# Kernel tuning notes

Measured on AMD Instinct MI355X. Metric: run time of the kernel, lower is better.

## Reference

```python
import jax, jax.numpy as jnp
import numpy as np

EMBED = 1024
HEADS = 16
HEAD_DIM = EMBED // HEADS
SCALE = HEAD_DIM ** -0.5


def setup_inputs() -> dict:
    key = jax.random.key(0)
    ks = jax.random.split(key, 9)
    B, N = 2, 2048
    std = EMBED ** -0.5
    return {
        "query": jax.random.normal(ks[0], (B, N, EMBED), jnp.float32),
        "key": jax.random.normal(ks[1], (B, N, EMBED), jnp.float32),
        "value": jax.random.normal(ks[2], (B, N, EMBED), jnp.float32),
        # torch nn.Linear weights are [out, in]; y = x @ W.T + b
        "Wq": jax.random.normal(ks[3], (EMBED, EMBED), jnp.float32) * std,
        "bq": jax.random.normal(ks[4], (EMBED,), jnp.float32) * 0.01,
        "Wk": jax.random.normal(ks[5], (EMBED, EMBED), jnp.float32) * std,
        "bk": jax.random.normal(ks[6], (EMBED,), jnp.float32) * 0.01,
        "Wv": jax.random.normal(ks[7], (EMBED, EMBED), jnp.float32) * std,
        "bv": jax.random.normal(ks[8], (EMBED,), jnp.float32) * 0.01,
    }


def reference(query, key, value, Wq, bq, Wk, bk, Wv, bv):
    B, NQ, _ = query.shape
    NK = key.shape[1]
    q = query @ Wq.T + bq  # [B, NQ, E]
    k = key @ Wk.T + bk    # [B, NK, E]
    v = value @ Wv.T + bv  # [B, NK, E]
    # split heads -> [B, H, N, Dh]
    q = q.reshape(B, NQ, HEADS, HEAD_DIM).transpose(0, 2, 1, 3)
    k = k.reshape(B, NK, HEADS, HEAD_DIM).transpose(0, 2, 1, 3)
    v = v.reshape(B, NK, HEADS, HEAD_DIM).transpose(0, 2, 1, 3)
    attn = jnp.einsum("bhqd,bhkd->bhqk", q, k) * SCALE  # [B, H, NQ, NK]
    attn = jax.nn.softmax(attn, axis=-1)
    out = jnp.einsum("bhqk,bhkd->bhqd", attn, v)  # [B, H, NQ, Dh]
    out = out.transpose(0, 2, 1, 3).reshape(B, NQ, EMBED)
    # o_proj is Identity (odim == embed_dim, o_proj=False); dropout is 0 (eval)
    return out
```

## Files before the change

### kernel.cpp

```cpp
#include <hip/hip_runtime.h>

#define EMB 1024
#define NSEQ 2048
#define NBATCH 2
#define NHEAD 16
#define DHEAD 64
#define QSCALE 0.18033688011112042f

typedef float f32x4 __attribute__((ext_vector_type(4)));
typedef short s16x8 __attribute__((ext_vector_type(8)));
typedef short s16x4 __attribute__((ext_vector_type(4)));

typedef __attribute__((address_space(3))) short lds_short;
typedef __attribute__((address_space(1))) const short glb_short;

__device__ __forceinline__ void gl_lds16(const short* g, short* l) {
    __builtin_amdgcn_global_load_lds((glb_short*)g, (lds_short*)l, 16, 0, 0);
}

__device__ __forceinline__ short bf16r(float f) {
    unsigned u = __float_as_uint(f);
    u += 0x7fffu + ((u >> 16) & 1u);
    return (short)(u >> 16);
}

__device__ __forceinline__ unsigned pkbf(float a, float b) {
#if defined(__has_builtin) && __has_builtin(__builtin_amdgcn_cvt_pk_bf16_f32)
    auto r = __builtin_amdgcn_cvt_pk_bf16_f32(a, b);
    unsigned u;
    __builtin_memcpy(&u, &r, 4);
    return u;
#else
    return ((unsigned)bf16r(a) & 0xffffu) | ((unsigned)bf16r(b) << 16);
#endif
}

__device__ __forceinline__ float fexp2(float x) {
#if defined(__has_builtin) && __has_builtin(__builtin_amdgcn_exp2f)
    return __builtin_amdgcn_exp2f(x);
#else
    return exp2f(x);
#endif
}

__global__ __launch_bounds__(256) void cvt6_kernel(
    const float* __restrict__ s0, const float* __restrict__ s1, const float* __restrict__ s2,
    const float* __restrict__ s3, const float* __restrict__ s4, const float* __restrict__ s5,
    short* __restrict__ d0, short* __restrict__ d1, short* __restrict__ d2,
    short* __restrict__ d3, short* __restrict__ d4, short* __restrict__ d5,
    int n0, int n1, int n2, int n3, int n4, int n5)
{
    const int seg = blockIdx.y;
    const float* s = (seg == 0) ? s0 : (seg == 1) ? s1 : (seg == 2) ? s2
                   : (seg == 3) ? s3 : (seg == 4) ? s4 : s5;
    short* d = (seg == 0) ? d0 : (seg == 1) ? d1 : (seg == 2) ? d2
             : (seg == 3) ? d3 : (seg == 4) ? d4 : d5;
    const int n = (seg == 0) ? n0 : (seg == 1) ? n1 : (seg == 2) ? n2
                : (seg == 3) ? n3 : (seg == 4) ? n4 : n5;

    const int i = (blockIdx.x * 256 + threadIdx.x) * 8;
    if (i >= n) return;
    float4 a = *(const float4*)(s + i);
    float4 b = *(const float4*)(s + i + 4);
    uint4 u = { pkbf(a.x, a.y), pkbf(a.z, a.w), pkbf(b.x, b.y), pkbf(b.z, b.w) };
    *(uint4*)(d + i) = u;
}

__global__ __launch_bounds__(256, 3) void proj2_kernel(
    const short* __restrict__ Xq, const short* __restrict__ Xk, const short* __restrict__ Xv,
    const short* __restrict__ Wq, const short* __restrict__ Wk, const short* __restrict__ Wv,
    const float* __restrict__ bq, const float* __restrict__ bk, const float* __restrict__ bv,
    short* __restrict__ Oq, short* __restrict__ Ok, short* __restrict__ Ov)
{
    const int z = blockIdx.z;
    const short* X    = (z == 0) ? Xq : (z == 1) ? Xk : Xv;
    const short* W    = (z == 0) ? Wq : (z == 1) ? Wk : Wv;
    const float* bias = (z == 0) ? bq : (z == 1) ? bk : bv;
    short* Out        = (z == 0) ? Oq : (z == 1) ? Ok : Ov;
    const float osc   = (z == 0) ? QSCALE : 1.0f;

    const int n0 = blockIdx.x * 128;
    const int m0 = blockIdx.y * 128;

    __shared__ __align__(16) short As[128 * 64];
    __shared__ __align__(16) short Bs[128 * 64];

    const int t    = threadIdx.x;
    const int lane = t & 63;
    const int wave = t >> 6;
    const int r    = lane & 15;
    const int quad = lane >> 4;
    const int wm   = (wave >> 1) * 64;
    const int wn   = (wave & 1) * 64;

    const int p0    = wave * 256 + lane;
    const int row0  = p0 >> 3;
    const int lc0   = (p0 & 7) ^ (row0 & 7);
    const short* gA = X + (size_t)(m0 + row0) * EMB + lc0 * 8;
    const short* gB = W + (size_t)(n0 + row0) * EMB + lc0 * 8;
    short* lA = As + p0 * 8;
    short* lB = Bs + p0 * 8;

    f32x4 acc[4][4];
#pragma unroll
    for (int i = 0; i < 4; ++i)
#pragma unroll
        for (int j = 0; j < 4; ++j)
#pragma unroll
            for (int v = 0; v < 4; ++v) acc[i][j][v] = 0.f;

    for (int k0 = 0; k0 < EMB; k0 += 64) {
#pragma unroll
        for (int i = 0; i < 4; ++i) {
            gl_lds16(gA + k0 + (size_t)8 * i * EMB, lA + i * 512);
            gl_lds16(gB + k0 + (size_t)8 * i * EMB, lB + i * 512);
        }
        __syncthreads();

#pragma unroll
        for (int ks = 0; ks < 2; ++ks) {
            const int fc = ((ks * 4 + quad) ^ (r & 7)) * 8;
            s16x8 af[4], bf[4];
#pragma unroll
            for (int i = 0; i < 4; ++i) af[i] = *(const s16x8*)&As[(wm + i * 16 + r) * 64 + fc];
#pragma unroll
            for (int j = 0; j < 4; ++j) bf[j] = *(const s16x8*)&Bs[(wn + j * 16 + r) * 64 + fc];
#pragma unroll
            for (int i = 0; i < 4; ++i)
#pragma unroll
                for (int j = 0; j < 4; ++j)
                    acc[i][j] = __builtin_amdgcn_mfma_f32_16x16x32_bf16(af[i], bf[j], acc[i][j], 0, 0, 0);
        }
        __syncthreads();
    }

#pragma unroll
    for (int j = 0; j < 4; ++j) {
        const int gn = n0 + wn + j * 16 + r;
        const float bb = bias[gn];
#pragma unroll
        for (int i = 0; i < 4; ++i)
#pragma unroll
            for (int reg = 0; reg < 4; ++reg) {
                const int gm = m0 + wm + i * 16 + quad * 4 + reg;
                Out[(size_t)gm * EMB + gn] = bf16r((acc[i][j][reg] + bb) * osc);
            }
    }
}

__global__ __launch_bounds__(256) void proj_kernel(
    const float* __restrict__ Xq, const float* __restrict__ Xk, const float* __restrict__ Xv,
    const float* __restrict__ Wq, const float* __restrict__ Wk, const float* __restrict__ Wv,
    const float* __restrict__ bq, const float* __restrict__ bk, const float* __restrict__ bv,
    short* __restrict__ Oq, short* __restrict__ Ok, short* __restrict__ Ov)
{
    const int z = blockIdx.z;
    const float* X    = (z == 0) ? Xq : (z == 1) ? Xk : Xv;
    const float* W    = (z == 0) ? Wq : (z == 1) ? Wk : Wv;
    const float* bias = (z == 0) ? bq : (z == 1) ? bk : bv;
    short* Out        = (z == 0) ? Oq : (z == 1) ? Ok : Ov;
    const float osc   = (z == 0) ? QSCALE : 1.0f;

    const int n0 = blockIdx.x * 128;
    const int m0 = blockIdx.y * 128;

    __shared__ __align__(16) short As[128][40];
    __shared__ __align__(16) short Bs[128][40];

    const int t    = threadIdx.x;
    const int lane = t & 63;
    const int wave = t >> 6;
    const int r    = lane & 15;
    const int quad = lane >> 4;
    const int wm   = (wave >> 1) * 64;
    const int wn   = (wave & 1) * 64;

    const int srow = t >> 1;
    const int scol = (t & 1) << 4;

    f32x4 acc[4][4];
#pragma unroll
    for (int i = 0; i < 4; ++i)
#pragma unroll
        for (int j = 0; j < 4; ++j)
#pragma unroll
            for (int v = 0; v < 4; ++v) acc[i][j][v] = 0.f;

    for (int k0 = 0; k0 < EMB; k0 += 32) {
        const float4* xp = (const float4*)(X + (size_t)(m0 + srow) * EMB + k0 + scol);
        const float4* wp = (const float4*)(W + (size_t)(n0 + srow) * EMB + k0 + scol);
        float4 x0 = xp[0], x1 = xp[1], x2 = xp[2], x3 = xp[3];
        float4 w0 = wp[0], w1 = wp[1], w2 = wp[2], w3 = wp[3];
        uint4 a0 = { pkbf(x0.x, x0.y), pkbf(x0.z, x0.w), pkbf(x1.x, x1.y), pkbf(x1.z, x1.w) };
        uint4 a1 = { pkbf(x2.x, x2.y), pkbf(x2.z, x2.w), pkbf(x3.x, x3.y), pkbf(x3.z, x3.w) };
        uint4 b0 = { pkbf(w0.x, w0.y), pkbf(w0.z, w0.w), pkbf(w1.x, w1.y), pkbf(w1.z, w1.w) };
        uint4 b1 = { pkbf(w2.x, w2.y), pkbf(w2.z, w2.w), pkbf(w3.x, w3.y), pkbf(w3.z, w3.w) };
        *(uint4*)&As[srow][scol]     = a0;
        *(uint4*)&As[srow][scol + 8] = a1;
        *(uint4*)&Bs[srow][scol]     = b0;
        *(uint4*)&Bs[srow][scol + 8] = b1;
        __syncthreads();

        s16x8 af[4], bf[4];
#pragma unroll
        for (int i = 0; i < 4; ++i) af[i] = *(const s16x8*)&As[wm + i * 16 + r][quad * 8];
#pragma unroll
        for (int j = 0; j < 4; ++j) bf[j] = *(const s16x8*)&Bs[wn + j * 16 + r][quad * 8];
#pragma unroll
        for (int i = 0; i < 4; ++i)
#pragma unroll
            for (int j = 0; j < 4; ++j)
                acc[i][j] = __builtin_amdgcn_mfma_f32_16x16x32_bf16(af[i], bf[j], acc[i][j], 0, 0, 0);
        __syncthreads();
    }

#pragma unroll
    for (int j = 0; j < 4; ++j) {
        const int gn = n0 + wn + j * 16 + r;
        const float bb = bias[gn];
#pragma unroll
        for (int i = 0; i < 4; ++i)
#pragma unroll
            for (int reg = 0; reg < 4; ++reg) {
                const int gm = m0 + wm + i * 16 + quad * 4 + reg;
                Out[(size_t)gm * EMB + gn] = bf16r((acc[i][j][reg] + bb) * osc);
            }
    }
}

__global__ __launch_bounds__(256) void vtrans_kernel(
    const short* __restrict__ Vp, short* __restrict__ VT)
{
    const int n0 = blockIdx.x * 64;
    const int h  = blockIdx.y;
    const int b  = blockIdx.z;
    __shared__ __align__(16) short L[64][72];

    const int t  = threadIdx.x;
    const int rr = t >> 2;
    const int cc = (t & 3) * 16;

    const short* src = Vp + (size_t)(b * NSEQ + n0 + rr) * EMB + h * DHEAD + cc;
    s16x8 a = *(const s16x8*)src;
    s16x8 c = *(const s16x8*)(src + 8);
    *(s16x8*)&L[rr][cc]     = a;
    *(s16x8*)&L[rr][cc + 8] = c;
    __syncthreads();

    const int d  = t >> 2;
    const int c4 = (t & 3) * 16;
    short vals[16];
#pragma unroll
    for (int i = 0; i < 16; ++i) vals[i] = L[c4 + i][d];
    short* dst = VT + ((size_t)(b * NHEAD + h) * DHEAD + d) * NSEQ + n0 + c4;
    *(s16x8*)dst       = *(s16x8*)&vals[0];
    *(s16x8*)(dst + 8) = *(s16x8*)&vals[8];
}

__global__ __launch_bounds__(256, 2) void attn7_kernel(
    const short* __restrict__ Qp, const short* __restrict__ Kp,
    const short* __restrict__ VT, float* __restrict__ Out)
{
    const int qblk = blockIdx.x * 128;
    const int h    = blockIdx.y;
    const int b    = blockIdx.z;

    __shared__ __align__(16) char smem[35840];
    short* Ks   = (short*)smem;
    short* Vs   = (short*)smem + 128 * 72;
    float* fbuf = (float*)smem;

    const int t    = threadIdx.x;
    const int lane = t & 63;
    const int w    = t >> 6;
    const int r    = lane & 15;
    const int quad = lane >> 4;

    const size_t rowbase = (size_t)b * NSEQ;
    const int    colbase = h * DHEAD;
    const size_t bh64    = (size_t)(b * NHEAD + h) * DHEAD;

    s16x8 qf[2][2];
#pragma unroll
    for (int qs = 0; qs < 2; ++qs)
#pragma unroll
        for (int ks = 0; ks < 2; ++ks)
            qf[qs][ks] = *(const s16x8*)(Qp + (rowbase + qblk + w * 32 + qs * 16 + r) * EMB
                                          + colbase + ks * 32 + quad * 8);

    f32x4 accO[2][4];
    float lsum[2] = {0.f, 0.f};
#pragma unroll
    for (int qs = 0; qs < 2; ++qs)
#pragma unroll
        for (int dt = 0; dt < 4; ++dt)
#pragma unroll
            for (int v = 0; v < 4; ++v) accO[qs][dt][v] = 0.f;

    const int srk = t >> 1;
    const int sck = (t & 1) * 32;
    const short* gK = Kp + (rowbase + srk) * EMB + colbase + sck;
    short* lK = Ks + srk * 72 + sck;

    const int srv = t >> 2;
    const int scv = (t & 3) * 32;
    const short* gV = VT + (bh64 + srv) * NSEQ + scv;
    short* lV = Vs + srv * 136 + scv;

    s16x8 kr[4], vr[4];
#pragma unroll
    for (int j = 0; j < 4; ++j) {
        kr[j] = *(const s16x8*)(gK + j * 8);
        vr[j] = *(const s16x8*)(gV + j * 8);
    }

    for (int kt = 0; kt < 16; ++kt) {
#pragma unroll
        for (int j = 0; j < 4; ++j) {
            *(s16x8*)(lK + j * 8) = kr[j];
            *(s16x8*)(lV + j * 8) = vr[j];
        }
        __syncthreads();

        if (kt + 1 < 16) {
            const short* gKt = gK + (size_t)(kt + 1) * 128 * EMB;
            const short* gVt = gV + (kt + 1) * 128;
#pragma unroll
            for (int j = 0; j < 4; ++j) {
                kr[j] = *(const s16x8*)(gKt + j * 8);
                vr[j] = *(const s16x8*)(gVt + j * 8);
            }
        }

        s16x8 pf[2][4];
#pragma unroll
        for (int s = 0; s < 4; ++s) {
            s16x8 kf00 = *(const s16x8*)&Ks[((2 * s) * 16 + r) * 72 + quad * 8];
            s16x8 kf01 = *(const s16x8*)&Ks[((2 * s) * 16 + r) * 72 + 32 + quad * 8];
            s16x8 kf10 = *(const s16x8*)&Ks[((2 * s + 1) * 16 + r) * 72 + quad * 8];
            s16x8 kf11 = *(const s16x8*)&Ks[((2 * s + 1) * 16 + r) * 72 + 32 + quad * 8];
#pragma unroll
            for (int qs = 0; qs < 2; ++qs) {
                f32x4 s0, s1;
#pragma unroll
                for (int v = 0; v < 4; ++v) { s0[v] = 0.f; s1[v] = 0.f; }
                s0 = __builtin_amdgcn_mfma_f32_16x16x32_bf16(kf00, qf[qs][0], s0, 0, 0, 0);
                s0 = __builtin_amdgcn_mfma_f32_16x16x32_bf16(kf01, qf[qs][1], s0, 0, 0, 0);
                s1 = __builtin_amdgcn_mfma_f32_16x16x32_bf16(kf10, qf[qs][0], s1, 0, 0, 0);
                s1 = __builtin_amdgcn_mfma_f32_16x16x32_bf16(kf11, qf[qs][1], s1, 0, 0, 0);
                float p0[4], p1[4];
#pragma unroll
                for (int reg = 0; reg < 4; ++reg) {
                    p0[reg] = fexp2(s0[reg]);
                    p1[reg] = fexp2(s1[reg]);
                    lsum[qs] += p0[reg] + p1[reg];
                }
                uint4 uu = { pkbf(p0[0], p0[1]), pkbf(p0[2], p0[3]),
                             pkbf(p1[0], p1[1]), pkbf(p1[2], p1[3]) };
                __builtin_memcpy(&pf[qs][s], &uu, 16);
            }
        }

#pragma unroll
        for (int dt = 0; dt < 4; ++dt) {
            s16x8 vfl[4];
#pragma unroll
            for (int s = 0; s < 4; ++s) {
                s16x4 lo = *(const s16x4*)&Vs[(dt * 16 + r) * 136 + s * 32 + quad * 4];
                s16x4 hi = *(const s16x4*)&Vs[(dt * 16 + r) * 136 + s * 32 + 16 + quad * 4];
                vfl[s] = __builtin_shufflevector(lo, hi, 0, 1, 2, 3, 4, 5, 6, 7);
            }
#pragma unroll
            for (int qs = 0; qs < 2; ++qs)
#pragma unroll
                for (int s = 0; s < 4; ++s)
                    accO[qs][dt] = __builtin_amdgcn_mfma_f32_16x16x32_bf16(vfl[s], pf[qs][s], accO[qs][dt], 0, 0, 0);
        }
        __syncthreads();
    }

    float rl[2];
#pragma unroll
    for (int qs = 0; qs < 2; ++qs) {
        float s = lsum[qs];
        s += __shfl_xor(s, 16);
        s += __shfl_xor(s, 32);
        rl[qs] = 1.f / s;
    }

#pragma unroll
    for (int qs = 0; qs < 2; ++qs) {
        __syncthreads();
#pragma unroll
        for (int dt = 0; dt < 4; ++dt)
#pragma unroll
            for (int reg = 0; reg < 4; ++reg)
                fbuf[(w * 16 + r) * 68 + dt * 16 + quad * 4 + reg] = accO[qs][dt][reg] * rl[qs];
        __syncthreads();
        const int qi   = t >> 2;
        const int c    = (t & 3) * 16;
        const int wsrc = qi >> 4;
        const int rsrc = qi & 15;
        const float4* fp = (const float4*)&fbuf[(wsrc * 16 + rsrc) * 68 + c];
        float4 o0 = fp[0], o1 = fp[1], o2 = fp[2], o3 = fp[3];
        float* op = Out + (rowbase + qblk + wsrc * 32 + qs * 16 + rsrc) * EMB + colbase + c;
        ((float4*)op)[0] = o0;
        ((float4*)op)[1] = o1;
        ((float4*)op)[2] = o2;
        ((float4*)op)[3] = o3;
    }
}

__global__ __launch_bounds__(256) void attn_fb_kernel(
    const short* __restrict__ Qp, const short* __restrict__ Kp,
    const short* __restrict__ Vp, float* __restrict__ Out)
{
    const int qt = blockIdx.x;
    const int h  = blockIdx.y;
    const int b  = blockIdx.z;

    __shared__ __align__(16) short Ks[64][72];
    __shared__ __align__(16) short VsT[64][72];
    __shared__ __align__(16) short Ps[4][16][72];

    const int t    = threadIdx.x;
    const int lane = t & 63;
    const int w    = t >> 6;
    const int r    = lane & 15;
    const int quad = lane >> 4;

    const size_t rowbase = (size_t)b * NSEQ;
    const int colbase    = h * DHEAD;

    const short* Qr = Qp + (rowbase + qt * 64 + w * 16 + r) * EMB + colbase;
    const s16x8 qf0 = *(const s16x8*)(Qr + quad * 8);
    const s16x8 qf1 = *(const s16x8*)(Qr + 32 + quad * 8);

    float mrow[4], lrow[4];
    f32x4 accO[4];
#pragma unroll
    for (int i = 0; i < 4; ++i) {
        mrow[i] = -INFINITY;
        lrow[i] = 0.f;
#pragma unroll
        for (int v = 0; v < 4; ++v) accO[i][v] = 0.f;
    }

    const int srow = t >> 2;
    const int scol = (t & 3) << 4;

    for (int kt = 0; kt < 32; ++kt) {
        const short* Krow = Kp + (rowbase + kt * 64 + srow) * EMB + colbase + scol;
        const short* Vrow = Vp + (rowbase + kt * 64 + srow) * EMB + colbase + scol;
        s16x8 kv0 = *(const s16x8*)Krow;
        s16x8 kv1 = *(const s16x8*)(Krow + 8);
        s16x8 vv0 = *(const s16x8*)Vrow;
        s16x8 vv1 = *(const s16x8*)(Vrow + 8);
        *(s16x8*)&Ks[srow][scol]     = kv0;
        *(s16x8*)&Ks[srow][scol + 8] = kv1;
#pragma unroll
        for (int i = 0; i < 8; ++i) {
            VsT[scol + i][srow]     = vv0[i];
            VsT[scol + 8 + i][srow] = vv1[i];
        }
        __syncthreads();

        f32x4 sacc[4];
#pragma unroll
        for (int j = 0; j < 4; ++j) {
#pragma unroll
            for (int v = 0; v < 4; ++v) sacc[j][v] = 0.f;
            s16x8 kf0 = *(const s16x8*)&Ks[j * 16 + r][quad * 8];
            s16x8 kf1 = *(const s16x8*)&Ks[j * 16 + r][32 + quad * 8];
            sacc[j] = __builtin_amdgcn_mfma_f32_16x16x32_bf16(qf0, kf0, sacc[j], 0, 0, 0);
            sacc[j] = __builtin_amdgcn_mfma_f32_16x16x32_bf16(qf1, kf1, sacc[j], 0, 0, 0);
        }

        float rmax[4];
#pragma unroll
        for (int reg = 0; reg < 4; ++reg) rmax[reg] = -INFINITY;
#pragma unroll
        for (int j = 0; j < 4; ++j)
#pragma unroll
            for (int reg = 0; reg < 4; ++reg)
                rmax[reg] = fmaxf(rmax[reg], sacc[j][reg]);
#pragma unroll
        for (int reg = 0; reg < 4; ++reg) {
#pragma unroll
            for (int mask = 1; mask <= 8; mask <<= 1)
                rmax[reg] = fmaxf(rmax[reg], __shfl_xor(rmax[reg], mask, 64));
        }

        float alpha[4], rsum[4];
#pragma unroll
        for (int reg = 0; reg < 4; ++reg) {
            float mnew = fmaxf(mrow[reg], rmax[reg]);
            alpha[reg] = fexp2(mrow[reg] - mnew);
            mrow[reg]  = mnew;
            rsum[reg]  = 0.f;
        }

#pragma unroll
        for (int j = 0; j < 4; ++j)
#pragma unroll
            for (int reg = 0; reg < 4; ++reg) {
                float p = fexp2(sacc[j][reg] - mrow[reg]);
                rsum[reg] += p;
                Ps[w][quad * 4 + reg][j * 16 + r] = bf16r(p);
            }
#pragma unroll
        for (int reg = 0; reg < 4; ++reg) {
#pragma unroll
            for (int mask = 1; mask <= 8; mask <<= 1)
                rsum[reg] += __shfl_xor(rsum[reg], mask, 64);
            lrow[reg] = lrow[reg] * alpha[reg] + rsum[reg];
        }
#pragma unroll
        for (int j = 0; j < 4; ++j)
#pragma unroll
            for (int reg = 0; reg < 4; ++reg) accO[j][reg] *= alpha[reg];

#pragma unroll
        for (int s = 0; s < 2; ++s) {
            s16x8 pfr = *(const s16x8*)&Ps[w][r][s * 32 + quad * 8];
#pragma unroll
            for (int j = 0; j < 4; ++j) {
                s16x8 vfr = *(const s16x8*)&VsT[j * 16 + r][s * 32 + quad * 8];
                accO[j] = __builtin_amdgcn_mfma_f32_16x16x32_bf16(pfr, vfr, accO[j], 0, 0, 0);
            }
        }
        __syncthreads();
    }

#pragma unroll
    for (int j = 0; j < 4; ++j)
#pragma unroll
        for (int reg = 0; reg < 4; ++reg) {
            const int qrow = qt * 64 + w * 16 + quad * 4 + reg;
            Out[(rowbase + qrow) * EMB + colbase + j * 16 + r] = accO[j][reg] / lrow[reg];
        }
}

extern "C" void kernel_launch(void* const* d_in, const int* in_sizes, int n_in,
                              void* d_out, int out_size, void* d_ws, size_t ws_size,
                              hipStream_t stream) {
    const float* query = (const float*)d_in[0];
    const float* key   = (const float*)d_in[1];
    const float* value = (const float*)d_in[2];
    const float* Wq    = (const float*)d_in[3];
    const float* bq    = (const float*)d_in[4];
    const float* Wk    = (const float*)d_in[5];
    const float* bk    = (const float*)d_in[6];
    const float* Wv    = (const float*)d_in[7];
    const float* bv    = (const float*)d_in[8];
    float* out = (float*)d_out;

    const size_t XBUF = (size_t)NBATCH * NSEQ * EMB;
    const size_t WBUF = (size_t)EMB * EMB;

    short* Qb  = (short*)d_ws;
    short* Kb  = Qb + XBUF;
    short* Vb  = Kb + XBUF;
    short* VTb = Vb + XBUF;
    short* Xqb = VTb + XBUF;
    short* Xkb = Xqb + XBUF;
    short* Xvb = Xkb + XBUF;
    short* Wqb = Xvb + XBUF;
    short* Wkb = Wqb + WBUF;
    short* Wvb = Wkb + WBUF;

    const size_t need_full  = (7 * XBUF + 3 * WBUF) * sizeof(short);
    const size_t need_attn7 = 4 * XBUF * sizeof(short);

    if (ws_size >= need_full) {
        cvt6_kernel<<<dim3(2048, 6), 256, 0, stream>>>(
            query, key, value, Wq, Wk, Wv,
            Xqb, Xkb, Xvb, Wqb, Wkb, Wvb,
            (int)XBUF, (int)XBUF, (int)XBUF, (int)WBUF, (int)WBUF, (int)WBUF);
        proj2_kernel<<<dim3(EMB / 128, (NBATCH * NSEQ) / 128, 3), 256, 0, stream>>>(
            Xqb, Xkb, Xvb, Wqb, Wkb, Wvb, bq, bk, bv, Qb, Kb, Vb);
        vtrans_kernel<<<dim3(NSEQ / 64, NHEAD, NBATCH), 256, 0, stream>>>(Vb, VTb);
        attn7_kernel<<<dim3(NSEQ / 128, NHEAD, NBATCH), 256, 0, stream>>>(Qb, Kb, VTb, out);
    } else if (ws_size >= need_attn7) {
        proj_kernel<<<dim3(EMB / 128, (NBATCH * NSEQ) / 128, 3), 256, 0, stream>>>(
            query, key, value, Wq, Wk, Wv, bq, bk, bv, Qb, Kb, Vb);
        vtrans_kernel<<<dim3(NSEQ / 64, NHEAD, NBATCH), 256, 0, stream>>>(Vb, VTb);
        attn7_kernel<<<dim3(NSEQ / 128, NHEAD, NBATCH), 256, 0, stream>>>(Qb, Kb, VTb, out);
    } else {
        proj_kernel<<<dim3(EMB / 128, (NBATCH * NSEQ) / 128, 3), 256, 0, stream>>>(
            query, key, value, Wq, Wk, Wv, bq, bk, bv, Qb, Kb, Vb);
        attn_fb_kernel<<<dim3(NSEQ / 64, NHEAD, NBATCH), 256, 0, stream>>>(Qb, Kb, Vb, out);
    }
}
```

Before: 205.5 us.

## Fuse V transpose into projection epilogue and widen attention blocks to 512 threads

The projection kernel now writes V directly in the per-head transposed layout, which removes the separate vtrans kernel launch and its extra pass over V. The attention kernel moves to 512 threads, with each wave handling 16 query rows instead of 32, and uses XOR-swizzled LDS layouts for K and V instead of padded rows. It also wraps MFMA groups in s_setprio. The epilogue is simplified to a single pass. The risks are scattered 8-byte stores in the projection epilogue and higher register and occupancy pressure from the 512-thread blocks.

```diff
diff --git a/kernel.cpp b/kernel.cpp
--- a/kernel.cpp
+++ b/kernel.cpp
@@ -134,17 +134,37 @@
         __syncthreads();
     }
 
-#pragma unroll
-    for (int j = 0; j < 4; ++j) {
-        const int gn = n0 + wn + j * 16 + r;
-        const float bb = bias[gn];
-#pragma unroll
-        for (int i = 0; i < 4; ++i)
-#pragma unroll
-            for (int reg = 0; reg < 4; ++reg) {
-                const int gm = m0 + wm + i * 16 + quad * 4 + reg;
-                Out[(size_t)gm * EMB + gn] = bf16r((acc[i][j][reg] + bb) * osc);
+    if (z != 2) {
+#pragma unroll
+        for (int j = 0; j < 4; ++j) {
+            const int gn = n0 + wn + j * 16 + r;
+            const float bb = bias[gn];
+#pragma unroll
+            for (int i = 0; i < 4; ++i)
+#pragma unroll
+                for (int reg = 0; reg < 4; ++reg) {
+                    const int gm = m0 + wm + i * 16 + quad * 4 + reg;
+                    Out[(size_t)gm * EMB + gn] = bf16r((acc[i][j][reg] + bb) * osc);
+                }
+        }
+    } else {
+#pragma unroll
+        for (int j = 0; j < 4; ++j) {
+            const int gn = n0 + wn + j * 16 + r;
+            const float bb = bias[gn];
+            const int hh = gn >> 6;
+            const int dd = gn & 63;
+#pragma unroll
+            for (int i = 0; i < 4; ++i) {
+                const int gm = m0 + wm + i * 16 + quad * 4;
+                const int bi = gm >> 11;
+                const int nn = gm & 2047;
+                s16x4 pk;
+#pragma unroll
+                for (int reg = 0; reg < 4; ++reg) pk[reg] = bf16r(acc[i][j][reg] + bb);
+                *(s16x4*)(Out + ((size_t)(bi * NHEAD + hh) * DHEAD + dd) * NSEQ + nn) = pk;
             }
+        }
     }
 }
 
@@ -257,7 +277,7 @@
     *(s16x8*)(dst + 8) = *(s16x8*)&vals[8];
 }
 
-__global__ __launch_bounds__(256, 2) void attn7_kernel(
+__global__ __launch_bounds__(512, 4) void attn8_kernel(
     const short* __restrict__ Qp, const short* __restrict__ Kp,
     const short* __restrict__ VT, float* __restrict__ Out)
 {
@@ -265,9 +285,9 @@
     const int h    = blockIdx.y;
     const int b    = blockIdx.z;
 
-    __shared__ __align__(16) char smem[35840];
+    __shared__ __align__(16) char smem[34816];
     short* Ks   = (short*)smem;
-    short* Vs   = (short*)smem + 128 * 72;
+    short* Vs   = (short*)smem + 128 * 64;
     float* fbuf = (float*)smem;
 
     const int t    = threadIdx.x;
@@ -275,140 +295,137 @@
     const int w    = t >> 6;
     const int r    = lane & 15;
     const int quad = lane >> 4;
+    const int r7   = r & 7;
 
     const size_t rowbase = (size_t)b * NSEQ;
     const int    colbase = h * DHEAD;
     const size_t bh64    = (size_t)(b * NHEAD + h) * DHEAD;
 
-    s16x8 qf[2][2];
-#pragma unroll
-    for (int qs = 0; qs < 2; ++qs)
-#pragma unroll
-        for (int ks = 0; ks < 2; ++ks)
-            qf[qs][ks] = *(const s16x8*)(Qp + (rowbase + qblk + w * 32 + qs * 16 + r) * EMB
-                                          + colbase + ks * 32 + quad * 8);
-
-    f32x4 accO[2][4];
-    float lsum[2] = {0.f, 0.f};
-#pragma unroll
-    for (int qs = 0; qs < 2; ++qs)
-#pragma unroll
-        for (int dt = 0; dt < 4; ++dt)
-#pragma unroll
-            for (int v = 0; v < 4; ++v) accO[qs][dt][v] = 0.f;
-
-    const int srk = t >> 1;
-    const int sck = (t & 1) * 32;
-    const short* gK = Kp + (rowbase + srk) * EMB + colbase + sck;
-    short* lK = Ks + srk * 72 + sck;
-
-    const int srv = t >> 2;
-    const int scv = (t & 3) * 32;
-    const short* gV = VT + (bh64 + srv) * NSEQ + scv;
-    short* lV = Vs + srv * 136 + scv;
-
-    s16x8 kr[4], vr[4];
-#pragma unroll
-    for (int j = 0; j < 4; ++j) {
-        kr[j] = *(const s16x8*)(gK + j * 8);
-        vr[j] = *(const s16x8*)(gV + j * 8);
-    }
+    const short* qrow = Qp + (rowbase + qblk + w * 16 + r) * EMB + colbase;
+    const s16x8 qf0 = *(const s16x8*)(qrow + quad * 8);
+    const s16x8 qf1 = *(const s16x8*)(qrow + 32 + quad * 8);
+
+    f32x4 accO[4];
+#pragma unroll
+    for (int dt = 0; dt < 4; ++dt)
+#pragma unroll
+        for (int v = 0; v < 4; ++v) accO[dt][v] = 0.f;
+    float lsum0 = 0.f, lsum1 = 0.f;
+    const f32x4 zf = {0.f, 0.f, 0.f, 0.f};
+
+    const int krow = t >> 2;
+    const int kc   = (t & 3) * 2;
+    const int kcs  = kc ^ (krow & 7);
+    const short* gK = Kp + (rowbase + krow) * EMB + colbase + kc * 8;
+    short* lK0 = Ks + krow * 64 + kcs * 8;
+    short* lK1 = Ks + krow * 64 + (kcs ^ 1) * 8;
+
+    const int vrow = t >> 3;
+    const int vc   = (t & 7) * 2;
+    const int vcs  = vc ^ (vrow & 7);
+    const short* gV = VT + (bh64 + vrow) * NSEQ + vc * 8;
+    short* lV0 = Vs + vrow * 128 + vcs * 8;
+    short* lV1 = Vs + vrow * 128 + (vcs ^ 1) * 8;
+
+    const int kofs = (quad ^ r7) * 8;
+    int vofs[4];
+    {
+        const int x4  = r7 & 4;
+        const int qr3 = ((quad >> 1) ^ r7) & 3;
+#pragma unroll
+        for (int s = 0; s < 4; ++s)
+            vofs[s] = ((((s << 2) ^ x4) | qr3) * 8) + (quad & 1) * 4;
+    }
+
+    s16x8 kr0 = *(const s16x8*)gK;
+    s16x8 kr1 = *(const s16x8*)(gK + 8);
+    s16x8 vr0 = *(const s16x8*)gV;
+    s16x8 vr1 = *(const s16x8*)(gV + 8);
+    const short* gKn = gK + (size_t)128 * EMB;
+    const short* gVn = gV + 128;
 
     for (int kt = 0; kt < 16; ++kt) {
-#pragma unroll
-        for (int j = 0; j < 4; ++j) {
-            *(s16x8*)(lK + j * 8) = kr[j];
-            *(s16x8*)(lV + j * 8) = vr[j];
-        }
+        *(s16x8*)lK0 = kr0;
+        *(s16x8*)lK1 = kr1;
+        *(s16x8*)lV0 = vr0;
+        *(s16x8*)lV1 = vr1;
         __syncthreads();
 
         if (kt + 1 < 16) {
-            const short* gKt = gK + (size_t)(kt + 1) * 128 * EMB;
-            const short* gVt = gV + (kt + 1) * 128;
-#pragma unroll
-            for (int j = 0; j < 4; ++j) {
-                kr[j] = *(const s16x8*)(gKt + j * 8);
-                vr[j] = *(const s16x8*)(gVt + j * 8);
+            kr0 = *(const s16x8*)gKn;
+            kr1 = *(const s16x8*)(gKn + 8);
+            vr0 = *(const s16x8*)gVn;
+            vr1 = *(const s16x8*)(gVn + 8);
+            gKn += (size_t)128 * EMB;
+            gVn += 128;
+        }
+
+        s16x8 pf[4];
+#pragma unroll
+        for (int s = 0; s < 4; ++s) {
+            const short* kb = Ks + (s * 32 + r) * 64;
+            const s16x8 kf00 = *(const s16x8*)(kb + kofs);
+            const s16x8 kf01 = *(const s16x8*)(kb + (kofs ^ 32));
+            const s16x8 kf10 = *(const s16x8*)(kb + 16 * 64 + kofs);
+            const s16x8 kf11 = *(const s16x8*)(kb + 16 * 64 + (kofs ^ 32));
+            __builtin_amdgcn_s_setprio(1);
+            f32x4 s0 = __builtin_amdgcn_mfma_f32_16x16x32_bf16(
+                kf01, qf1, __builtin_amdgcn_mfma_f32_16x16x32_bf16(kf00, qf0, zf, 0, 0, 0), 0, 0, 0);
+            f32x4 s1 = __builtin_amdgcn_mfma_f32_16x16x32_bf16(
+                kf11, qf1, __builtin_amdgcn_mfma_f32_16x16x32_bf16(kf10, qf0, zf, 0, 0, 0), 0, 0, 0);
+            __builtin_amdgcn_s_setprio(0);
+            float p0[4], p1[4];
+#pragma unroll
+            for (int reg = 0; reg < 4; ++reg) {
+                p0[reg] = fexp2(s0[reg]);
+                p1[reg] = fexp2(s1[reg]);
+                lsum0 += p0[reg];
+                lsum1 += p1[reg];
             }
-        }
-
-        s16x8 pf[2][4];
-#pragma unroll
-        for (int s = 0; s < 4; ++s) {
-            s16x8 kf00 = *(const s16x8*)&Ks[((2 * s) * 16 + r) * 72 + quad * 8];
-            s16x8 kf01 = *(const s16x8*)&Ks[((2 * s) * 16 + r) * 72 + 32 + quad * 8];
-            s16x8 kf10 = *(const s16x8*)&Ks[((2 * s + 1) * 16 + r) * 72 + quad * 8];
-            s16x8 kf11 = *(const s16x8*)&Ks[((2 * s + 1) * 16 + r) * 72 + 32 + quad * 8];
-#pragma unroll
-            for (int qs = 0; qs < 2; ++qs) {
-                f32x4 s0, s1;
-#pragma unroll
-                for (int v = 0; v < 4; ++v) { s0[v] = 0.f; s1[v] = 0.f; }
-                s0 = __builtin_amdgcn_mfma_f32_16x16x32_bf16(kf00, qf[qs][0], s0, 0, 0, 0);
-                s0 = __builtin_amdgcn_mfma_f32_16x16x32_bf16(kf01, qf[qs][1], s0, 0, 0, 0);
-                s1 = __builtin_amdgcn_mfma_f32_16x16x32_bf16(kf10, qf[qs][0], s1, 0, 0, 0);
-                s1 = __builtin_amdgcn_mfma_f32_16x16x32_bf16(kf11, qf[qs][1], s1, 0, 0, 0);
-                float p0[4], p1[4];
-#pragma unroll
-                for (int reg = 0; reg < 4; ++reg) {
-                    p0[reg] = fexp2(s0[reg]);
-                    p1[reg] = fexp2(s1[reg]);
-                    lsum[qs] += p0[reg] + p1[reg];
-                }
-                uint4 uu = { pkbf(p0[0], p0[1]), pkbf(p0[2], p0[3]),
-                             pkbf(p1[0], p1[1]), pkbf(p1[2], p1[3]) };
-                __builtin_memcpy(&pf[qs][s], &uu, 16);
-            }
+            uint4 uu = { pkbf(p0[0], p0[1]), pkbf(p0[2], p0[3]),
+                         pkbf(p1[0], p1[1]), pkbf(p1[2], p1[3]) };
+            __builtin_memcpy(&pf[s], &uu, 16);
         }
 
 #pragma unroll
         for (int dt = 0; dt < 4; ++dt) {
+            const short* vb = Vs + (dt * 16 + r) * 128;
             s16x8 vfl[4];
 #pragma unroll
             for (int s = 0; s < 4; ++s) {
-                s16x4 lo = *(const s16x4*)&Vs[(dt * 16 + r) * 136 + s * 32 + quad * 4];
-                s16x4 hi = *(const s16x4*)&Vs[(dt * 16 + r) * 136 + s * 32 + 16 + quad * 4];
+                s16x4 lo = *(const s16x4*)(vb + vofs[s]);
+                s16x4 hi = *(const s16x4*)(vb + (vofs[s] ^ 16));
                 vfl[s] = __builtin_shufflevector(lo, hi, 0, 1, 2, 3, 4, 5, 6, 7);
             }
-#pragma unroll
-            for (int qs = 0; qs < 2; ++qs)
-#pragma unroll
-                for (int s = 0; s < 4; ++s)
-                    accO[qs][dt] = __builtin_amdgcn_mfma_f32_16x16x32_bf16(vfl[s], pf[qs][s], accO[qs][dt], 0, 0, 0);
-        }
-        __syncthreads();
-    }
-
-    float rl[2];
-#pragma unroll
-    for (int qs = 0; qs < 2; ++qs) {
-        float s = lsum[qs];
-        s += __shfl_xor(s, 16);
-        s += __shfl_xor(s, 32);
-        rl[qs] = 1.f / s;
-    }
-
-#pragma unroll
-    for (int qs = 0; qs < 2; ++qs) {
-        __syncthreads();
-#pragma unroll
-        for (int dt = 0; dt < 4; ++dt)
-#pragma unroll
-            for (int reg = 0; reg < 4; ++reg)
-                fbuf[(w * 16 + r) * 68 + dt * 16 + quad * 4 + reg] = accO[qs][dt][reg] * rl[qs];
-        __syncthreads();
-        const int qi   = t >> 2;
-        const int c    = (t & 3) * 16;
-        const int wsrc = qi >> 4;
-        const int rsrc = qi & 15;
-        const float4* fp = (const float4*)&fbuf[(wsrc * 16 + rsrc) * 68 + c];
-        float4 o0 = fp[0], o1 = fp[1], o2 = fp[2], o3 = fp[3];
-        float* op = Out + (rowbase + qblk + wsrc * 32 + qs * 16 + rsrc) * EMB + colbase + c;
-        ((float4*)op)[0] = o0;
-        ((float4*)op)[1] = o1;
-        ((float4*)op)[2] = o2;
-        ((float4*)op)[3] = o3;
-    }
+            __builtin_amdgcn_s_setprio(1);
+#pragma unroll
+            for (int s = 0; s < 4; ++s)
+                accO[dt] = __builtin_amdgcn_mfma_f32_16x16x32_bf16(vfl[s], pf[s], accO[dt], 0, 0, 0);
+            __builtin_amdgcn_s_setprio(0);
+        }
+        __syncthreads();
+    }
+
+    float ls = lsum0 + lsum1;
+    ls += __shfl_xor(ls, 16);
+    ls += __shfl_xor(ls, 32);
+    const float rl = 1.f / ls;
+
+#pragma unroll
+    for (int dt = 0; dt < 4; ++dt)
+#pragma unroll
+        for (int reg = 0; reg < 4; ++reg)
+            fbuf[(w * 16 + r) * 68 + dt * 16 + quad * 4 + reg] = accO[dt][reg] * rl;
+    __syncthreads();
+    const int qi = t >> 2;
+    const int c  = (t & 3) * 16;
+    const float4* fp = (const float4*)&fbuf[qi * 68 + c];
+    float4 o0 = fp[0], o1 = fp[1], o2 = fp[2], o3 = fp[3];
+    float* op = Out + (rowbase + qblk + qi) * EMB + colbase + c;
+    ((float4*)op)[0] = o0;
+    ((float4*)op)[1] = o1;
+    ((float4*)op)[2] = o2;
+    ((float4*)op)[3] = o3;
 }
 
 __global__ __launch_bounds__(256) void attn_fb_kernel(
@@ -570,7 +587,7 @@
     short* Wvb = Wkb + WBUF;
 
     const size_t need_full  = (7 * XBUF + 3 * WBUF) * sizeof(short);
-    const size_t need_attn7 = 4 * XBUF * sizeof(short);
+    const size_t need_attn8 = 4 * XBUF * sizeof(short);
 
     if (ws_size >= need_full) {
         cvt6_kernel<<<dim3(2048, 6), 256, 0, stream>>>(
@@ -578,14 +595,13 @@
             Xqb, Xkb, Xvb, Wqb, Wkb, Wvb,
             (int)XBUF, (int)XBUF, (int)XBUF, (int)WBUF, (int)WBUF, (int)WBUF);
         proj2_kernel<<<dim3(EMB / 128, (NBATCH * NSEQ) / 128, 3), 256, 0, stream>>>(
-            Xqb, Xkb, Xvb, Wqb, Wkb, Wvb, bq, bk, bv, Qb, Kb, Vb);
-        vtrans_kernel<<<dim3(NSEQ / 64, NHEAD, NBATCH), 256, 0, stream>>>(Vb, VTb);
-        attn7_kernel<<<dim3(NSEQ / 128, NHEAD, NBATCH), 256, 0, stream>>>(Qb, Kb, VTb, out);
-    } else if (ws_size >= need_attn7) {
+            Xqb, Xkb, Xvb, Wqb, Wkb, Wvb, bq, bk, bv, Qb, Kb, VTb);
+        attn8_kernel<<<dim3(NSEQ / 128, NHEAD, NBATCH), 512, 0, stream>>>(Qb, Kb, VTb, out);
+    } else if (ws_size >= need_attn8) {
         proj_kernel<<<dim3(EMB / 128, (NBATCH * NSEQ) / 128, 3), 256, 0, stream>>>(
             query, key, value, Wq, Wk, Wv, bq, bk, bv, Qb, Kb, Vb);
         vtrans_kernel<<<dim3(NSEQ / 64, NHEAD, NBATCH), 256, 0, stream>>>(Vb, VTb);
-        attn7_kernel<<<dim3(NSEQ / 128, NHEAD, NBATCH), 256, 0, stream>>>(Qb, Kb, VTb, out);
+        attn8_kernel<<<dim3(NSEQ / 128, NHEAD, NBATCH), 512, 0, stream>>>(Qb, Kb, VTb, out);
     } else {
         proj_kernel<<<dim3(EMB / 128, (NBATCH * NSEQ) / 128, 3), 256, 0, stream>>>(
             query, key, value, Wq, Wk, Wv, bq, bk, bv, Qb, Kb, Vb);
```

New measurement: 207.7 us. About the same (+1.1%).
